# Kernel optimization log

Measured on AMD Instinct MI355X. Metric: run time of the kernel, lower is better.

The kernel has to match this reference:

```python
import jax, jax.numpy as jnp
import numpy as np


def setup_inputs() -> dict:
    key = jax.random.key(0)
    ks = jax.random.split(key, 6)
    B, O, L, D, D2 = 32, 1, 2048, 1024, 512
    query = jax.random.normal(ks[0], (B, O, D), dtype=jnp.float32)
    context = jax.random.normal(ks[1], (B, L, D), dtype=jnp.float32)
    W_in = jax.random.normal(ks[2], (D, D), dtype=jnp.float32) * (1.0 / np.sqrt(D))
    W_out = jax.random.normal(ks[3], (D2, 2 * D), dtype=jnp.float32) * (1.0 / np.sqrt(2 * D))
    ae = jax.random.uniform(ks[4], (B, 1, 1), dtype=jnp.float32)
    ab = jax.random.uniform(ks[5], (B, 1, 1), dtype=jnp.float32)
    return {"query": query, "context": context, "W_in": W_in, "W_out": W_out, "ae": ae, "ab": ab}


def reference(query, context, W_in, W_out, ae, ab):
    B, O, D = query.shape  # O == 1 (required by the broadcast in mix)
    L = context.shape[1]
    # linear_in (no bias): q @ W_in^T
    q = jnp.einsum('bod,ed->boe', query, W_in)  # [B,1,D]
    # attention scores + softmax over key dimension
    scores = jnp.einsum('bod,bld->bol', q, context)  # [B,1,L]
    attn = jax.nn.softmax(scores, axis=-1)  # [B,1,L]
    # mix: weights broadcast against context^T -> [B,D,L]
    mix = attn * jnp.transpose(context, (0, 2, 1))
    # temporal decay bias: delta_t = [L-1, ..., 0]
    delta_t = jnp.arange(L - 1, -1, -1, dtype=jnp.float32).reshape(1, 1, L)
    bt = jnp.exp(-ab * delta_t)  # [B,1,L]
    term_2 = jax.nn.relu(ae * mix * bt)  # [B,D,L]
    mixed = jnp.sum(term_2 + mix, axis=-1)[:, None, :]  # [B,1,D]
    combined = jnp.concatenate([mixed, q], axis=2)  # [B,1,2D]
    out = jnp.tanh(jnp.einsum('boc,ec->boe', combined, W_out))  # [B,1,D2]
    return (out, attn)
```

## Files before the change

kernel.cpp:

```cpp
#include <hip/hip_runtime.h>
#include <hip/hip_bf16.h>
#include <math.h>

#define NB 32
#define NL 2048
#define ND 1024
#define ND2 512
#define CH 32
#define ROWS (NL / CH)
#define RPW (ROWS / 4)

__device__ __forceinline__ float waveReduceSumAll(float v) {
    for (int off = 32; off > 0; off >>= 1) v += __shfl_xor(v, off, 64);
    return v;
}
__device__ __forceinline__ float waveReduceSum(float v) {
    for (int off = 32; off > 0; off >>= 1) v += __shfl_down(v, off, 64);
    return v;
}

__global__ __launch_bounds__(256) void k_qproj(const float* __restrict__ query,
                                               const float* __restrict__ W_in,
                                               float* __restrict__ q) {
    int wave = blockIdx.x * 4 + (threadIdx.x >> 6);
    int lane = threadIdx.x & 63;
    int b = wave >> 10;
    int e = wave & 1023;
    const float4* qr = (const float4*)(query + (size_t)b * ND) + lane * 4;
    const float4* wr = (const float4*)(W_in + (size_t)e * ND) + lane * 4;
    float s = 0.f;
#pragma unroll
    for (int t = 0; t < 4; t++) {
        float4 a = qr[t], w = wr[t];
        s += a.x * w.x + a.y * w.y + a.z * w.z + a.w * w.w;
    }
    s = waveReduceSum(s);
    if (lane == 0) q[b * ND + e] = s;
}

__global__ __launch_bounds__(256) void k_flash(const float* __restrict__ q,
                                               const float* __restrict__ ctx,
                                               const float* __restrict__ ae,
                                               const float* __restrict__ ab,
                                               float* __restrict__ scores,
                                               float* __restrict__ pm,
                                               float* __restrict__ pZ,
                                               float* __restrict__ pacc) {
    int b = blockIdx.x >> 5;
    int chunk = blockIdx.x & 31;
    int wave = threadIdx.x >> 6;
    int lane = threadIdx.x & 63;

    const float4* qp = (const float4*)(q + (size_t)b * ND) + lane * 4;
    float4 q0 = qp[0], q1 = qp[1], q2 = qp[2], q3 = qp[3];
    float aev = ae[b], abv = ab[b];

    float m = -INFINITY, Z = 0.f;
    float acc[16];
#pragma unroll
    for (int j = 0; j < 16; j++) acc[j] = 0.f;

    int l0 = chunk * ROWS + wave * RPW;
    for (int i = 0; i < RPW; i++) {
        int l = l0 + i;
        const float4* cp = (const float4*)(ctx + ((size_t)b * NL + l) * ND) + lane * 4;
        float4 c0 = cp[0], c1 = cp[1], c2 = cp[2], c3 = cp[3];
        float s = c0.x*q0.x + c0.y*q0.y + c0.z*q0.z + c0.w*q0.w
                + c1.x*q1.x + c1.y*q1.y + c1.z*q1.z + c1.w*q1.w
                + c2.x*q2.x + c2.y*q2.y + c2.z*q2.z + c2.w*q2.w
                + c3.x*q3.x + c3.y*q3.y + c3.z*q3.z + c3.w*q3.w;
        s = waveReduceSumAll(s);
        if (lane == 0) scores[b * NL + l] = s;

        float bt = __expf(-abv * (float)(NL - 1 - l));
        if (s > m) {
            float sc = __expf(m - s);
            m = s;
            Z *= sc;
#pragma unroll
            for (int j = 0; j < 16; j++) acc[j] *= sc;
        }
        float p = __expf(s - m);
        float k2 = p * aev * bt;
        Z += p;
        float c[16] = {c0.x,c0.y,c0.z,c0.w, c1.x,c1.y,c1.z,c1.w,
                       c2.x,c2.y,c2.z,c2.w, c3.x,c3.y,c3.z,c3.w};
#pragma unroll
        for (int j = 0; j < 16; j++)
            acc[j] += p * c[j] + k2 * fmaxf(c[j], 0.f);
    }

    __shared__ float sacc[4 * ND];
    __shared__ float sm[4], sZ[4];
#pragma unroll
    for (int j = 0; j < 16; j++) sacc[wave * ND + lane * 16 + j] = acc[j];
    if (lane == 0) { sm[wave] = m; sZ[wave] = Z; }
    __syncthreads();

    int tid = threadIdx.x;
    float m0 = sm[0], m1 = sm[1], m2 = sm[2], m3 = sm[3];
    float mb = fmaxf(fmaxf(m0, m1), fmaxf(m2, m3));
    float e0 = __expf(m0 - mb), e1 = __expf(m1 - mb),
          e2 = __expf(m2 - mb), e3 = __expf(m3 - mb);
    int d = tid * 4;
    float4 v;
    v.x = e0*sacc[0*ND+d+0] + e1*sacc[1*ND+d+0] + e2*sacc[2*ND+d+0] + e3*sacc[3*ND+d+0];
    v.y = e0*sacc[0*ND+d+1] + e1*sacc[1*ND+d+1] + e2*sacc[2*ND+d+1] + e3*sacc[3*ND+d+1];
    v.z = e0*sacc[0*ND+d+2] + e1*sacc[1*ND+d+2] + e2*sacc[2*ND+d+2] + e3*sacc[3*ND+d+2];
    v.w = e0*sacc[0*ND+d+3] + e1*sacc[1*ND+d+3] + e2*sacc[2*ND+d+3] + e3*sacc[3*ND+d+3];
    *(float4*)(pacc + ((size_t)(b * CH + chunk)) * ND + d) = v;
    if (tid == 0) {
        pm[b * CH + chunk] = mb;
        pZ[b * CH + chunk] = e0*sZ[0] + e1*sZ[1] + e2*sZ[2] + e3*sZ[3];
    }
}

__global__ __launch_bounds__(256) void k_merge(const float* __restrict__ pm,
                                               const float* __restrict__ pZ,
                                               const float* __restrict__ pacc,
                                               const float* __restrict__ scores,
                                               float* __restrict__ mixed,
                                               float* __restrict__ attn_out) {
    int b = blockIdx.x;
    int tid = threadIdx.x;
    __shared__ float ew[CH];
    __shared__ float smg, sinvZ;
    if (tid == 0) {
        float mg = -INFINITY;
        for (int i = 0; i < CH; i++) mg = fmaxf(mg, pm[b * CH + i]);
        float Zg = 0.f;
        for (int i = 0; i < CH; i++) Zg += __expf(pm[b * CH + i] - mg) * pZ[b * CH + i];
        smg = mg; sinvZ = 1.f / Zg;
    }
    __syncthreads();
    float mg = smg, invZ = sinvZ;
    if (tid < CH) ew[tid] = __expf(pm[b * CH + tid] - mg);
    __syncthreads();

    int d = tid * 4;
    float4 accv = {0.f, 0.f, 0.f, 0.f};
    for (int i = 0; i < CH; i++) {
        float4 pv = *(const float4*)(pacc + ((size_t)(b * CH + i)) * ND + d);
        float e = ew[i];
        accv.x += e * pv.x; accv.y += e * pv.y;
        accv.z += e * pv.z; accv.w += e * pv.w;
    }
    accv.x *= invZ; accv.y *= invZ; accv.z *= invZ; accv.w *= invZ;
    *(float4*)(mixed + (size_t)b * ND + d) = accv;

    for (int l = tid; l < NL; l += 256)
        attn_out[b * NL + l] = __expf(scores[b * NL + l] - mg) * invZ;
}

__global__ __launch_bounds__(256) void k_out(const float* __restrict__ mixed,
                                             const float* __restrict__ q,
                                             const float* __restrict__ W_out,
                                             float* __restrict__ out) {
    int wave = blockIdx.x * 4 + (threadIdx.x >> 6);
    int lane = threadIdx.x & 63;
    int b = wave >> 9;
    int e = wave & 511;
    int c0 = lane * 32;
    const float* src = (lane < 32) ? (mixed + (size_t)b * ND + c0)
                                   : (q + (size_t)b * ND + c0 - ND);
    const float4* wr = (const float4*)(W_out + (size_t)e * 2 * ND + c0);
    const float4* sp = (const float4*)src;
    float s = 0.f;
#pragma unroll
    for (int t = 0; t < 8; t++) {
        float4 w = wr[t], x = sp[t];
        s += w.x * x.x + w.y * x.y + w.z * x.z + w.w * x.w;
    }
    s = waveReduceSum(s);
    if (lane == 0) out[b * ND2 + e] = tanhf(s);
}

extern "C" void kernel_launch(void* const* d_in, const int* in_sizes, int n_in,
                              void* d_out, int out_size, void* d_ws, size_t ws_size,
                              hipStream_t stream) {
    const float* query = (const float*)d_in[0];
    const float* ctx   = (const float*)d_in[1];
    const float* W_in  = (const float*)d_in[2];
    const float* W_out = (const float*)d_in[3];
    const float* ae    = (const float*)d_in[4];
    const float* ab    = (const float*)d_in[5];
    float* out = (float*)d_out;
    float* attn_out = out + (size_t)NB * ND2;

    float* ws     = (float*)d_ws;
    float* q      = ws;
    float* scores = ws + 32768;
    float* pm     = ws + 98304;
    float* pZ     = ws + 99328;
    float* pacc   = ws + 100352;
    float* mixed  = ws + 1148928;

    k_qproj<<<8192, 256, 0, stream>>>(query, W_in, q);
    k_flash<<<NB * CH, 256, 0, stream>>>(q, ctx, ae, ab, scores, pm, pZ, pacc);
    k_merge<<<NB, 256, 0, stream>>>(pm, pZ, pacc, scores, mixed, attn_out);
    k_out<<<4096, 256, 0, stream>>>(mixed, q, W_out, out);
}
```

Before: 429.0 us.

## Reuse W_in rows across batches in q-projection and stream context nontemporally

The q-projection kernel now has each wave keep one W_in row in registers and loop over all 32 batch queries, which are staged through shared memory in two halves. Previously every (batch, row) pair reloaded its W_in row, so W_in was read 32 times; now it is read once. The grid shrinks from 8192 to 256 blocks, which lowers parallelism for this small kernel. Separately, the context reads in the flash kernel use nontemporal loads so the single-use streaming data does not pollute the cache.

```diff
diff --git a/kernel.cpp b/kernel.cpp
--- a/kernel.cpp
+++ b/kernel.cpp
@@ -10,6 +10,8 @@
 #define ROWS (NL / CH)
 #define RPW (ROWS / 4)
 
+typedef float f4v __attribute__((ext_vector_type(4)));
+
 __device__ __forceinline__ float waveReduceSumAll(float v) {
     for (int off = 32; off > 0; off >>= 1) v += __shfl_xor(v, off, 64);
     return v;
@@ -22,20 +24,44 @@
 __global__ __launch_bounds__(256) void k_qproj(const float* __restrict__ query,
                                                const float* __restrict__ W_in,
                                                float* __restrict__ q) {
-    int wave = blockIdx.x * 4 + (threadIdx.x >> 6);
-    int lane = threadIdx.x & 63;
-    int b = wave >> 10;
-    int e = wave & 1023;
-    const float4* qr = (const float4*)(query + (size_t)b * ND) + lane * 4;
+    __shared__ float sq[16 * ND];
+    int tid = threadIdx.x;
+    int wave = tid >> 6, lane = tid & 63;
+    int e = blockIdx.x * 4 + wave;
     const float4* wr = (const float4*)(W_in + (size_t)e * ND) + lane * 4;
-    float s = 0.f;
-#pragma unroll
-    for (int t = 0; t < 4; t++) {
-        float4 a = qr[t], w = wr[t];
-        s += a.x * w.x + a.y * w.y + a.z * w.z + a.w * w.w;
-    }
-    s = waveReduceSum(s);
-    if (lane == 0) q[b * ND + e] = s;
+    float4 w0 = wr[0], w1 = wr[1], w2 = wr[2], w3 = wr[3];
+
+    for (int half = 0; half < 2; half++) {
+        __syncthreads();
+        const float4* qsrc = (const float4*)(query + (size_t)half * 16 * ND);
+        float4* qdst = (float4*)sq;
+        for (int i = tid; i < 16 * ND / 4; i += 256) qdst[i] = qsrc[i];
+        __syncthreads();
+        for (int g = 0; g < 4; g++) {
+            float p[4];
+#pragma unroll
+            for (int bb = 0; bb < 4; bb++) {
+                const float4* qp = (const float4*)(sq + (g * 4 + bb) * ND) + lane * 4;
+                float4 a0 = qp[0], a1 = qp[1], a2 = qp[2], a3 = qp[3];
+                p[bb] = a0.x*w0.x + a0.y*w0.y + a0.z*w0.z + a0.w*w0.w
+                      + a1.x*w1.x + a1.y*w1.y + a1.z*w1.z + a1.w*w1.w
+                      + a2.x*w2.x + a2.y*w2.y + a2.z*w2.z + a2.w*w2.w
+                      + a3.x*w3.x + a3.y*w3.y + a3.z*w3.z + a3.w*w3.w;
+            }
+#pragma unroll
+            for (int off = 32; off > 0; off >>= 1) {
+                p[0] += __shfl_down(p[0], off, 64);
+                p[1] += __shfl_down(p[1], off, 64);
+                p[2] += __shfl_down(p[2], off, 64);
+                p[3] += __shfl_down(p[3], off, 64);
+            }
+            if (lane == 0) {
+                int b0 = half * 16 + g * 4;
+#pragma unroll
+                for (int bb = 0; bb < 4; bb++) q[(b0 + bb) * ND + e] = p[bb];
+            }
+        }
+    }
 }
 
 __global__ __launch_bounds__(256) void k_flash(const float* __restrict__ q,
@@ -63,8 +89,11 @@
     int l0 = chunk * ROWS + wave * RPW;
     for (int i = 0; i < RPW; i++) {
         int l = l0 + i;
-        const float4* cp = (const float4*)(ctx + ((size_t)b * NL + l) * ND) + lane * 4;
-        float4 c0 = cp[0], c1 = cp[1], c2 = cp[2], c3 = cp[3];
+        const f4v* cp = (const f4v*)(ctx + ((size_t)b * NL + l) * ND) + lane * 4;
+        f4v c0 = __builtin_nontemporal_load(cp + 0);
+        f4v c1 = __builtin_nontemporal_load(cp + 1);
+        f4v c2 = __builtin_nontemporal_load(cp + 2);
+        f4v c3 = __builtin_nontemporal_load(cp + 3);
         float s = c0.x*q0.x + c0.y*q0.y + c0.z*q0.z + c0.w*q0.w
                 + c1.x*q1.x + c1.y*q1.y + c1.z*q1.z + c1.w*q1.w
                 + c2.x*q2.x + c2.y*q2.y + c2.z*q2.z + c2.w*q2.w
@@ -195,7 +224,7 @@
     float* pacc   = ws + 100352;
     float* mixed  = ws + 1148928;
 
-    k_qproj<<<8192, 256, 0, stream>>>(query, W_in, q);
+    k_qproj<<<256, 256, 0, stream>>>(query, W_in, q);
     k_flash<<<NB * CH, 256, 0, stream>>>(q, ctx, ae, ab, scores, pm, pZ, pacc);
     k_merge<<<NB, 256, 0, stream>>>(pm, pZ, pacc, scores, mixed, attn_out);
     k_out<<<4096, 256, 0, stream>>>(mixed, q, W_out, out);
```

Result: no change. 432.8 us (+0.9%).
